# Kernel optimization log

Hardware: AMD Instinct MI355X
Metric: run time of the kernel (lower is better)

Reference implementation:

```python
import jax, jax.numpy as jnp
import numpy as np

B, S, DIM, H = 2, 2048, 1024, 16
DK = DIM // H  # 64
NEG = -10000000000.0


def setup_inputs() -> dict:
    key = jax.random.key(0)
    k1, k2, k3, k4, k5, k6 = jax.random.split(key, 6)
    dec_xs = jax.random.normal(k1, (B, S, DIM), dtype=jnp.float32)
    enc_xs = jax.random.normal(k2, (B, S, DIM), dtype=jnp.float32)
    mask = jax.random.randint(k3, (B, S, S), 0, 2, dtype=jnp.int32)
    # torch Linear weights: out = x @ W.T, bias=False
    sc = 1.0 / np.sqrt(DIM)
    Wq = jax.random.normal(k4, (DIM, DIM), dtype=jnp.float32) * sc
    Wkv = jax.random.normal(k5, (2 * DIM, DIM), dtype=jnp.float32) * sc
    Wo = jax.random.normal(k6, (DIM, DIM), dtype=jnp.float32) * sc
    return {"dec_xs": dec_xs, "enc_xs": enc_xs, "Wq": Wq, "Wkv": Wkv, "Wo": Wo, "mask": mask}


def reference(dec_xs, enc_xs, Wq, Wkv, Wo, mask):
    b, s, dim = enc_xs.shape
    qs = dec_xs @ Wq.T                      # [b,s,dim]  (dropout inactive in eval)
    kv = enc_xs @ Wkv.T                     # [b,s,2*dim]
    ks, vs = jnp.split(kv, 2, axis=-1)
    # head layout: view(b, s, dk, h) -- heads LAST, as in the original
    qs = qs.reshape(b, s, DK, H)
    ks = ks.reshape(b, s, DK, H)
    vs = vs.reshape(b, s, DK, H)
    scores = jnp.einsum('bqdh,bkdh->bqkh', qs, ks) / np.sqrt(DK)
    scores = jnp.where(mask[..., None] == 0, NEG, scores)
    weights = jax.nn.softmax(scores, axis=-2)  # softmax over key axis
    out = jnp.einsum('bqkh,bkdh->bqdh', weights, vs).reshape(b, s, dim)
    return out @ Wo.T
```

## Files before the change

### kernel.cpp

```cpp
#include <hip/hip_runtime.h>
#include <hip/hip_bf16.h>

#define BB 2
#define SS 2048
#define DIMM 1024
#define HH 16
#define DKK 64
#define QSCALE 0.18033688011112042592f

using bf16 = __hip_bfloat16;
typedef __attribute__((ext_vector_type(8))) short v8s;
typedef __attribute__((ext_vector_type(4))) short v4s;
typedef __attribute__((ext_vector_type(4))) float f32x4;
typedef __attribute__((ext_vector_type(16))) float f32x16;

__device__ __forceinline__ void cvt4(const float* __restrict__ s,
                                     bf16* __restrict__ d, int idx) {
  const float4 f = ((const float4*)s)[idx];
  bf16 t[4] = {__float2bfloat16(f.x), __float2bfloat16(f.y),
               __float2bfloat16(f.z), __float2bfloat16(f.w)};
  *(v4s*)(d + (size_t)idx * 4) = *(const v4s*)t;
}

__device__ __forceinline__ int cvt_pk_bf16(float lo, float hi) {
  int r;
  asm("v_cvt_pk_bf16_f32 %0, %1, %2" : "=v"(r) : "v"(lo), "v"(hi));
  return r;
}

__global__ __launch_bounds__(256) void convert_pack_kernel(
    const float* __restrict__ dec, const float* __restrict__ enc,
    const float* __restrict__ Wq, const float* __restrict__ Wkv,
    const float* __restrict__ Wo, const int* __restrict__ mask,
    bf16* __restrict__ decb, bf16* __restrict__ encb, bf16* __restrict__ Wqb,
    bf16* __restrict__ Wkvb, bf16* __restrict__ Wob,
    unsigned long long* __restrict__ mp) {
  const int gid = blockIdx.x * 256 + threadIdx.x;
  const int NT = 256 * 1024;
#pragma unroll
  for (int i = 0; i < 4; ++i) cvt4(dec, decb, gid + i * NT);
#pragma unroll
  for (int i = 0; i < 4; ++i) cvt4(enc, encb, gid + i * NT);
  cvt4(Wq, Wqb, gid);
#pragma unroll
  for (int i = 0; i < 2; ++i) cvt4(Wkv, Wkvb, gid + i * NT);
  {
    const int n = gid >> 8;
    const int c4 = (gid & 255) * 4;
    const int h = c4 >> 6, d0 = c4 & 63;
    const float* src = Wo + (size_t)n * DIMM + h;
    bf16 t[4];
#pragma unroll
    for (int i2 = 0; i2 < 4; ++i2)
      t[i2] = __float2bfloat16(src[(d0 + i2) * 16]);
    *(v4s*)(Wob + (size_t)n * DIMM + c4) = *(const v4s*)t;
  }
  const int lane = threadIdx.x & 63;
  const int wave_id = gid >> 6;
  for (int i = 0; i < 32; ++i) {
    const size_t w = (size_t)wave_id * 32 + i;
    const unsigned long long bm = __ballot(mask[w * 64 + lane] != 0);
    if (lane == 0) {
      const int bb = (int)(w >> 16);
      const int qq = (int)((w >> 5) & 2047);
      const int kc = (int)(w & 31);
      mp[((size_t)bb * 32 + kc) * SS + qq] = bm;
    }
  }
}

__global__ __launch_bounds__(256) void proj_gemm_kernel(
    const bf16* __restrict__ decb, const bf16* __restrict__ encb,
    const bf16* __restrict__ Wqb, const bf16* __restrict__ Wkvb,
    bf16* __restrict__ Qr, bf16* __restrict__ Kr, bf16* __restrict__ Vt) {
  __shared__ __align__(16) bf16 As[128][72];
  __shared__ __align__(16) bf16 Bs[128][72];
  const int t = threadIdx.x;
  const int wave = t >> 6, lane = t & 63;
  const int quad = lane >> 4, l15 = lane & 15;
  const int wm = (wave >> 1) * 64, wn = (wave & 1) * 64;
  const int bx = blockIdx.x;
  const int kind = bx >> 3;
  const int g = bx & 7;
  const int m0 = blockIdx.y * 128;

  const int sr = t >> 2;
  const int sc = (t & 3) * 16;
  const int voff = (kind == 2) ? DIMM : 0;
  const int wr0 = sr * 16 + g * 2 + voff;
  const int wr1 = sr * 16 + g * 2 + 1 + voff;

  const bf16* arow0;
  const bf16* arow1;
  const bf16* brow0;
  const bf16* brow1;
  if (kind == 0) {
    arow0 = decb + (size_t)(m0 + sr) * DIMM;
    arow1 = decb + (size_t)(m0 + sr + 64) * DIMM;
    brow0 = Wqb + (size_t)wr0 * DIMM;
    brow1 = Wqb + (size_t)wr1 * DIMM;
  } else if (kind == 1) {
    arow0 = encb + (size_t)(m0 + sr) * DIMM;
    arow1 = encb + (size_t)(m0 + sr + 64) * DIMM;
    brow0 = Wkvb + (size_t)wr0 * DIMM;
    brow1 = Wkvb + (size_t)wr1 * DIMM;
  } else {
    arow0 = Wkvb + (size_t)wr0 * DIMM;
    arow1 = Wkvb + (size_t)wr1 * DIMM;
    brow0 = encb + (size_t)(m0 + sr) * DIMM;
    brow1 = encb + (size_t)(m0 + sr + 64) * DIMM;
  }

  v8s apf[4], bpf[4];
  auto loadAB = [&](int kc) {
    apf[0] = ((const v8s*)(arow0 + kc + sc))[0];
    apf[1] = ((const v8s*)(arow0 + kc + sc))[1];
    apf[2] = ((const v8s*)(arow1 + kc + sc))[0];
    apf[3] = ((const v8s*)(arow1 + kc + sc))[1];
    bpf[0] = ((const v8s*)(brow0 + kc + sc))[0];
    bpf[1] = ((const v8s*)(brow0 + kc + sc))[1];
    bpf[2] = ((const v8s*)(brow1 + kc + sc))[0];
    bpf[3] = ((const v8s*)(brow1 + kc + sc))[1];
  };

  f32x4 acc[4][4] = {};
  loadAB(0);

  for (int kc = 0; kc < DIMM; kc += 64) {
    __syncthreads();
    *(v8s*)&As[sr][sc] = apf[0];
    *(v8s*)&As[sr][sc + 8] = apf[1];
    *(v8s*)&As[sr + 64][sc] = apf[2];
    *(v8s*)&As[sr + 64][sc + 8] = apf[3];
    *(v8s*)&Bs[sr][sc] = bpf[0];
    *(v8s*)&Bs[sr][sc + 8] = bpf[1];
    *(v8s*)&Bs[sr + 64][sc] = bpf[2];
    *(v8s*)&Bs[sr + 64][sc + 8] = bpf[3];
    if (kc + 64 < DIMM) loadAB(kc + 64);
    __syncthreads();
#pragma unroll
    for (int ks = 0; ks < 2; ++ks) {
      v8s af[4], bfr[4];
#pragma unroll
      for (int i = 0; i < 4; ++i)
        af[i] = *(const v8s*)&As[wm + i * 16 + l15][ks * 32 + quad * 8];
#pragma unroll
      for (int j = 0; j < 4; ++j)
        bfr[j] = *(const v8s*)&Bs[wn + j * 16 + l15][ks * 32 + quad * 8];
#pragma unroll
      for (int i = 0; i < 4; ++i)
#pragma unroll
        for (int j = 0; j < 4; ++j)
          acc[i][j] = __builtin_amdgcn_mfma_f32_16x16x32_bf16(
              af[i], bfr[j], acc[i][j], 0, 0, 0);
    }
  }

#pragma unroll
  for (int i = 0; i < 4; ++i) {
#pragma unroll
    for (int r = 0; r < 4; ++r) {
      const int mm = wm + i * 16 + quad * 4 + r;
#pragma unroll
      for (int j = 0; j < 4; ++j) {
        const int nn = wn + j * 16 + l15;
        const float v = acc[i][j][r];
        if (kind == 0) {
          Qr[(size_t)(m0 + mm) * DIMM + g * 128 + nn] =
              __float2bfloat16(v * QSCALE);
        } else if (kind == 1) {
          Kr[(size_t)(m0 + mm) * DIMM + g * 128 + nn] = __float2bfloat16(v);
        } else {
          const int h = g * 2 + (mm >> 6), d = mm & 63;
          const int sn = m0 + nn;
          const int b = sn >> 11, s = sn & (SS - 1);
          Vt[(((size_t)b * HH + h) * DKK + d) * SS + s] = __float2bfloat16(v);
        }
      }
    }
  }
}

__global__ __launch_bounds__(256) void out_gemm_kernel(
    const bf16* __restrict__ A, const bf16* __restrict__ W,
    float* __restrict__ out) {
  __shared__ __align__(16) bf16 As[128][72];
  __shared__ __align__(16) bf16 Bs[64][72];
  const int t = threadIdx.x;
  const int wave = t >> 6, lane = t & 63;
  const int quad = lane >> 4, l15 = lane & 15;
  const int wm = (wave >> 1) * 64, wn = (wave & 1) * 32;
  const int n0 = blockIdx.x * 64;
  const int m0 = blockIdx.y * 128;
  const int sr = t >> 2;
  const int sc = (t & 3) * 16;

  v8s ar[4], br[2];
  auto loadA = [&](int kc) {
#pragma unroll
    for (int rr = 0; rr < 2; ++rr) {
      const bf16* p = A + (size_t)(m0 + sr + rr * 64) * DIMM + kc + sc;
#pragma unroll
      for (int i = 0; i < 2; ++i) ar[rr * 2 + i] = ((const v8s*)p)[i];
    }
  };
  auto loadB = [&](int kc) {
    const bf16* p = W + (size_t)(n0 + sr) * DIMM + kc + sc;
#pragma unroll
    for (int i = 0; i < 2; ++i) br[i] = ((const v8s*)p)[i];
  };

  f32x4 acc[4][2] = {};
  loadA(0);
  loadB(0);
  for (int kc = 0; kc < DIMM; kc += 64) {
    __syncthreads();
#pragma unroll
    for (int rr = 0; rr < 2; ++rr) {
      *(v8s*)&As[sr + rr * 64][sc] = ar[rr * 2 + 0];
      *(v8s*)&As[sr + rr * 64][sc + 8] = ar[rr * 2 + 1];
    }
    *(v8s*)&Bs[sr][sc] = br[0];
    *(v8s*)&Bs[sr][sc + 8] = br[1];
    if (kc + 64 < DIMM) {
      loadA(kc + 64);
      loadB(kc + 64);
    }
    __syncthreads();
#pragma unroll
    for (int ks = 0; ks < 2; ++ks) {
      v8s af[4], bfr[2];
#pragma unroll
      for (int i = 0; i < 4; ++i)
        af[i] = *(const v8s*)&As[wm + i * 16 + l15][ks * 32 + quad * 8];
#pragma unroll
      for (int j = 0; j < 2; ++j)
        bfr[j] = *(const v8s*)&Bs[wn + j * 16 + l15][ks * 32 + quad * 8];
#pragma unroll
      for (int i = 0; i < 4; ++i)
#pragma unroll
        for (int j = 0; j < 2; ++j)
          acc[i][j] = __builtin_amdgcn_mfma_f32_16x16x32_bf16(
              af[i], bfr[j], acc[i][j], 0, 0, 0);
    }
  }

#pragma unroll
  for (int i = 0; i < 4; ++i) {
#pragma unroll
    for (int r = 0; r < 4; ++r) {
      const int m = m0 + wm + i * 16 + quad * 4 + r;
#pragma unroll
      for (int j = 0; j < 2; ++j) {
        const int n = n0 + wn + j * 16 + l15;
        out[(size_t)m * DIMM + n] = acc[i][j][r];
      }
    }
  }
}

__global__ __launch_bounds__(256) void attn_kernel(
    const bf16* __restrict__ Qr, const bf16* __restrict__ Kr,
    const bf16* __restrict__ Vt, const unsigned long long* __restrict__ mp,
    bf16* __restrict__ Ar) {
  __shared__ __align__(16) bf16 Ks[2][64][72];
  __shared__ __align__(16) bf16 Vs[2][64][72];

  const int t = threadIdx.x;
  const int wave = t >> 6, lane = t & 63;
  const int l31 = lane & 31, hf = lane >> 5;

  const int bx = blockIdx.x;
  const int xcd = bx & 7, j = bx >> 3;
  const int g = (xcd << 2) | (j & 3);
  const int tile = j >> 2;
  const int hd = g & 15, b = g >> 4;

  const int qw = tile * 128 + wave * 32;
  const size_t bhv = ((size_t)b * HH + hd) * DKK;

  v8s bq[4];
  {
    const bf16* qrow = Qr + ((size_t)(b * SS + qw + l31)) * DIMM + hd * 64;
#pragma unroll
    for (int cs = 0; cs < 4; ++cs)
      bq[cs] = *(const v8s*)(qrow + cs * 16 + 8 * hf);
  }

  v8s vones;
#pragma unroll
  for (int i = 0; i < 8; ++i) vones[i] = (short)0x3F80;

  f32x16 o0 = {}, o1 = {}, ol = {};

  const int r0 = t >> 2;
  const int c0 = (t & 3) * 16;

  auto loadK = [&](int kt, v8s* kr) {
    const bf16* p =
        Kr + ((size_t)(b * SS + kt * 64 + r0)) * DIMM + hd * 64 + c0;
    kr[0] = ((const v8s*)p)[0];
    kr[1] = ((const v8s*)p)[1];
  };
  auto loadV = [&](int kt, v8s* vr) {
    const bf16* p = Vt + (bhv + r0) * SS + kt * 64 + c0;
    vr[0] = ((const v8s*)p)[0];
    vr[1] = ((const v8s*)p)[1];
  };
  auto loadM = [&](int kt) {
    return mp[((size_t)b * 32 + kt) * SS + qw + l31];
  };

  v8s kreg[2], vreg[2];
  loadK(0, kreg);
  loadV(0, vreg);
  *(v8s*)&Ks[0][r0][c0] = kreg[0];
  *(v8s*)&Ks[0][r0][c0 + 8] = kreg[1];
  *(v8s*)&Vs[0][r0][c0] = vreg[0];
  *(v8s*)&Vs[0][r0][c0 + 8] = vreg[1];
  loadK(1, kreg);
  loadV(1, vreg);
  unsigned long long mwcur = loadM(0);

  int p = 0;
  for (int kt = 0; kt < 32; ++kt) {
    __syncthreads();
    if (kt < 31) {
      *(v8s*)&Ks[p ^ 1][r0][c0] = kreg[0];
      *(v8s*)&Ks[p ^ 1][r0][c0 + 8] = kreg[1];
      *(v8s*)&Vs[p ^ 1][r0][c0] = vreg[0];
      *(v8s*)&Vs[p ^ 1][r0][c0 + 8] = vreg[1];
      if (kt < 30) {
        loadK(kt + 2, kreg);
        loadV(kt + 2, vreg);
      }
    }
    unsigned long long mwnext = (kt < 31) ? loadM(kt + 1) : 0ULL;
    const unsigned long long mq = mwcur >> (4 * hf);

    f32x16 st[2];
#pragma unroll
    for (int n = 0; n < 2; ++n) {
      f32x16 s = {};
#pragma unroll
      for (int cs = 0; cs < 4; ++cs) {
        const v8s ak = *(const v8s*)&Ks[p][n * 32 + l31][cs * 16 + 8 * hf];
        s = __builtin_amdgcn_mfma_f32_32x32x16_bf16(ak, bq[cs], s, 0, 0, 0);
      }
      st[n] = s;
    }

    int pd[8][2];
#pragma unroll
    for (int n = 0; n < 2; ++n)
#pragma unroll
      for (int g2 = 0; g2 < 4; ++g2)
#pragma unroll
        for (int jj = 0; jj < 2; ++jj) {
          const int bp = 32 * n + 8 * g2 + 2 * jj;
          const int m = g2 * 4 + 2 * jj;
          const float p0 = ((mq >> bp) & 1)
                               ? __builtin_amdgcn_exp2f(st[n][m])
                               : 0.f;
          const float p1 = ((mq >> (bp + 1)) & 1)
                               ? __builtin_amdgcn_exp2f(st[n][m + 1])
                               : 0.f;
          pd[n * 4 + g2][jj] = cvt_pk_bf16(p0, p1);
        }

    v8s af[4];
#pragma unroll
    for (int ks = 0; ks < 4; ++ks) {
      int a0 = pd[2 * ks][0], b0 = pd[2 * ks + 1][0];
      int a1 = pd[2 * ks][1], b1 = pd[2 * ks + 1][1];
      asm("v_permlane32_swap_b32 %0, %1" : "+v"(a0), "+v"(b0));
      asm("v_permlane32_swap_b32 %0, %1" : "+v"(a1), "+v"(b1));
      int4 w;
      w.x = a0;
      w.y = a1;
      w.z = b0;
      w.w = b1;
      af[ks] = *(v8s*)&w;
    }

#pragma unroll
    for (int ks = 0; ks < 4; ++ks) {
      const v8s bv0 = *(const v8s*)&Vs[p][l31][ks * 16 + 8 * hf];
      const v8s bv1 = *(const v8s*)&Vs[p][32 + l31][ks * 16 + 8 * hf];
      o0 = __builtin_amdgcn_mfma_f32_32x32x16_bf16(af[ks], bv0, o0, 0, 0, 0);
      o1 = __builtin_amdgcn_mfma_f32_32x32x16_bf16(af[ks], bv1, o1, 0, 0, 0);
      ol = __builtin_amdgcn_mfma_f32_32x32x16_bf16(af[ks], vones, ol, 0, 0, 0);
    }
    mwcur = mwnext;
    p ^= 1;
  }

#pragma unroll
  for (int m = 0; m < 16; ++m) {
    const float inv = __builtin_amdgcn_rcpf(ol[m]);
    const int q = qw + (m & 3) + 8 * (m >> 2) + 4 * hf;
    const size_t row = (size_t)b * SS + q;
    Ar[row * DIMM + hd * 64 + l31] = __float2bfloat16(o0[m] * inv);
    Ar[row * DIMM + hd * 64 + 32 + l31] = __float2bfloat16(o1[m] * inv);
  }
}

extern "C" void kernel_launch(void* const* d_in, const int* in_sizes, int n_in,
                              void* d_out, int out_size, void* d_ws,
                              size_t ws_size, hipStream_t stream) {
  const float* dec = (const float*)d_in[0];
  const float* enc = (const float*)d_in[1];
  const float* Wq = (const float*)d_in[2];
  const float* Wkv = (const float*)d_in[3];
  const float* Wo = (const float*)d_in[4];
  const int* mask = (const int*)d_in[5];
  float* out = (float*)d_out;

  bf16* decb = (bf16*)d_out;
  bf16* Wqb = (bf16*)((char*)d_out + ((size_t)2 * SS * DIMM * 2));

  char* ws = (char*)d_ws;
  size_t off = 0;
  bf16* encb = (bf16*)(ws + off);
  bf16* Ar = (bf16*)(ws + off);   off += (size_t)2 * SS * DIMM * 2;
  bf16* Wkvb = (bf16*)(ws + off); off += (size_t)2 * DIMM * DIMM * 2;
  bf16* Wob = (bf16*)(ws + off);  off += (size_t)DIMM * DIMM * 2;
  bf16* Qr = (bf16*)(ws + off);   off += (size_t)2 * SS * DIMM * 2;
  bf16* Kr = (bf16*)(ws + off);   off += (size_t)2 * SS * DIMM * 2;
  bf16* Vt = (bf16*)(ws + off);   off += (size_t)2 * SS * DIMM * 2;
  unsigned long long* mp = (unsigned long long*)(ws + off);

  dim3 blk(256);
  convert_pack_kernel<<<dim3(1024), blk, 0, stream>>>(
      dec, enc, Wq, Wkv, Wo, mask, decb, encb, Wqb, Wkvb, Wob, mp);
  proj_gemm_kernel<<<dim3(24, 32), blk, 0, stream>>>(decb, encb, Wqb, Wkvb, Qr,
                                                     Kr, Vt);
  attn_kernel<<<dim3(512), dim3(256), 0, stream>>>(Qr, Kr, Vt, mp, Ar);
  out_gemm_kernel<<<dim3(16, 32), blk, 0, stream>>>(Ar, Wob, out);
}
```

Measured before the change: 245.2 us.

## Split attention key loop across two wave groups and merge partial sums in LDS

Doubles the attention block to 512 threads: waves 0-3 and 4-7 handle even and odd 64-key tiles, each pair of tiles staged together in a double-buffered LDS layout. After the loop, the upper waves write their partial O and row-sum accumulators to shared memory, and the lower waves add them before normalising and storing. This is meant to raise the number of waves per CU and hide latency in a grid of only 512 blocks. The cost is doubled LDS per block, an extra reduction step with two barriers, and fewer registers available per thread.

New measurement: 240.1 us. 2.1% less time.

```diff
diff --git a/kernel.cpp b/kernel.cpp
--- a/kernel.cpp
+++ b/kernel.cpp
@@ -259,16 +259,17 @@
   }
 }
 
-__global__ __launch_bounds__(256) void attn_kernel(
+__global__ __launch_bounds__(512) void attn_kernel(
     const bf16* __restrict__ Qr, const bf16* __restrict__ Kr,
     const bf16* __restrict__ Vt, const unsigned long long* __restrict__ mp,
     bf16* __restrict__ Ar) {
-  __shared__ __align__(16) bf16 Ks[2][64][72];
-  __shared__ __align__(16) bf16 Vs[2][64][72];
+  __shared__ __align__(16) bf16 smem[2][2][2][64][72];
 
   const int t = threadIdx.x;
   const int wave = t >> 6, lane = t & 63;
   const int l31 = lane & 31, hf = lane >> 5;
+  const int qb = wave & 3;
+  const int pr = wave >> 2;
 
   const int bx = blockIdx.x;
   const int xcd = bx & 7, j = bx >> 3;
@@ -276,7 +277,7 @@
   const int tile = j >> 2;
   const int hd = g & 15, b = g >> 4;
 
-  const int qw = tile * 128 + wave * 32;
+  const int qw = tile * 128 + qb * 32;
   const size_t bhv = ((size_t)b * HH + hd) * DKK;
 
   v8s bq[4];
@@ -293,61 +294,64 @@
 
   f32x16 o0 = {}, o1 = {}, ol = {};
 
-  const int r0 = t >> 2;
-  const int c0 = (t & 3) * 16;
-
-  auto loadK = [&](int kt, v8s* kr) {
-    const bf16* p =
-        Kr + ((size_t)(b * SS + kt * 64 + r0)) * DIMM + hd * 64 + c0;
-    kr[0] = ((const v8s*)p)[0];
-    kr[1] = ((const v8s*)p)[1];
-  };
-  auto loadV = [&](int kt, v8s* vr) {
-    const bf16* p = Vt + (bhv + r0) * SS + kt * 64 + c0;
-    vr[0] = ((const v8s*)p)[0];
-    vr[1] = ((const v8s*)p)[1];
+  const int r0 = t >> 3;
+  const int c0 = (t & 7) * 8;
+
+  auto gK = [&](int kt) {
+    return *(const v8s*)(Kr + ((size_t)(b * SS + kt * 64 + r0)) * DIMM +
+                         hd * 64 + c0);
+  };
+  auto gV = [&](int kt) {
+    return *(const v8s*)(Vt + (bhv + r0) * SS + kt * 64 + c0);
   };
   auto loadM = [&](int kt) {
     return mp[((size_t)b * 32 + kt) * SS + qw + l31];
   };
 
-  v8s kreg[2], vreg[2];
-  loadK(0, kreg);
-  loadV(0, vreg);
-  *(v8s*)&Ks[0][r0][c0] = kreg[0];
-  *(v8s*)&Ks[0][r0][c0 + 8] = kreg[1];
-  *(v8s*)&Vs[0][r0][c0] = vreg[0];
-  *(v8s*)&Vs[0][r0][c0 + 8] = vreg[1];
-  loadK(1, kreg);
-  loadV(1, vreg);
-  unsigned long long mwcur = loadM(0);
-
-  int p = 0;
-  for (int kt = 0; kt < 32; ++kt) {
+  {
+    const v8s k0 = gK(0), v0 = gV(0), k1 = gK(1), v1 = gV(1);
+    *(v8s*)&smem[0][0][0][r0][c0] = k0;
+    *(v8s*)&smem[1][0][0][r0][c0] = v0;
+    *(v8s*)&smem[0][1][0][r0][c0] = k1;
+    *(v8s*)&smem[1][1][0][r0][c0] = v1;
+  }
+  v8s kpr[2], vpr[2];
+  kpr[0] = gK(2);
+  vpr[0] = gV(2);
+  kpr[1] = gK(3);
+  vpr[1] = gV(3);
+  unsigned long long mwcur = loadM(pr);
+
+  for (int s = 0; s < 16; ++s) {
     __syncthreads();
-    if (kt < 31) {
-      *(v8s*)&Ks[p ^ 1][r0][c0] = kreg[0];
-      *(v8s*)&Ks[p ^ 1][r0][c0 + 8] = kreg[1];
-      *(v8s*)&Vs[p ^ 1][r0][c0] = vreg[0];
-      *(v8s*)&Vs[p ^ 1][r0][c0 + 8] = vreg[1];
-      if (kt < 30) {
-        loadK(kt + 2, kreg);
-        loadV(kt + 2, vreg);
+    const int nb = (s + 1) & 1;
+    if (s < 15) {
+      *(v8s*)&smem[0][0][nb][r0][c0] = kpr[0];
+      *(v8s*)&smem[1][0][nb][r0][c0] = vpr[0];
+      *(v8s*)&smem[0][1][nb][r0][c0] = kpr[1];
+      *(v8s*)&smem[1][1][nb][r0][c0] = vpr[1];
+      if (s < 14) {
+        kpr[0] = gK(2 * s + 4);
+        vpr[0] = gV(2 * s + 4);
+        kpr[1] = gK(2 * s + 5);
+        vpr[1] = gV(2 * s + 5);
       }
     }
-    unsigned long long mwnext = (kt < 31) ? loadM(kt + 1) : 0ULL;
+    const unsigned long long mwnext = (s < 15) ? loadM(2 * s + 2 + pr) : 0ULL;
     const unsigned long long mq = mwcur >> (4 * hf);
+    const int cb = s & 1;
 
     f32x16 st[2];
 #pragma unroll
     for (int n = 0; n < 2; ++n) {
-      f32x16 s = {};
+      f32x16 sa = {};
 #pragma unroll
       for (int cs = 0; cs < 4; ++cs) {
-        const v8s ak = *(const v8s*)&Ks[p][n * 32 + l31][cs * 16 + 8 * hf];
-        s = __builtin_amdgcn_mfma_f32_32x32x16_bf16(ak, bq[cs], s, 0, 0, 0);
+        const v8s ak =
+            *(const v8s*)&smem[0][pr][cb][n * 32 + l31][cs * 16 + 8 * hf];
+        sa = __builtin_amdgcn_mfma_f32_32x32x16_bf16(ak, bq[cs], sa, 0, 0, 0);
       }
-      st[n] = s;
+      st[n] = sa;
     }
 
     int pd[8][2];
@@ -359,12 +363,11 @@
         for (int jj = 0; jj < 2; ++jj) {
           const int bp = 32 * n + 8 * g2 + 2 * jj;
           const int m = g2 * 4 + 2 * jj;
-          const float p0 = ((mq >> bp) & 1)
-                               ? __builtin_amdgcn_exp2f(st[n][m])
-                               : 0.f;
-          const float p1 = ((mq >> (bp + 1)) & 1)
-                               ? __builtin_amdgcn_exp2f(st[n][m + 1])
-                               : 0.f;
+          const float p0 =
+              ((mq >> bp) & 1) ? __builtin_amdgcn_exp2f(st[n][m]) : 0.f;
+          const float p1 =
+              ((mq >> (bp + 1)) & 1) ? __builtin_amdgcn_exp2f(st[n][m + 1])
+                                     : 0.f;
           pd[n * 4 + g2][jj] = cvt_pk_bf16(p0, p1);
         }
 
@@ -385,23 +388,47 @@
 
 #pragma unroll
     for (int ks = 0; ks < 4; ++ks) {
-      const v8s bv0 = *(const v8s*)&Vs[p][l31][ks * 16 + 8 * hf];
-      const v8s bv1 = *(const v8s*)&Vs[p][32 + l31][ks * 16 + 8 * hf];
+      const v8s bv0 = *(const v8s*)&smem[1][pr][cb][l31][ks * 16 + 8 * hf];
+      const v8s bv1 =
+          *(const v8s*)&smem[1][pr][cb][32 + l31][ks * 16 + 8 * hf];
       o0 = __builtin_amdgcn_mfma_f32_32x32x16_bf16(af[ks], bv0, o0, 0, 0, 0);
       o1 = __builtin_amdgcn_mfma_f32_32x32x16_bf16(af[ks], bv1, o1, 0, 0, 0);
       ol = __builtin_amdgcn_mfma_f32_32x32x16_bf16(af[ks], vones, ol, 0, 0, 0);
     }
     mwcur = mwnext;
-    p ^= 1;
-  }
-
-#pragma unroll
-  for (int m = 0; m < 16; ++m) {
-    const float inv = __builtin_amdgcn_rcpf(ol[m]);
-    const int q = qw + (m & 3) + 8 * (m >> 2) + 4 * hf;
-    const size_t row = (size_t)b * SS + q;
-    Ar[row * DIMM + hd * 64 + l31] = __float2bfloat16(o0[m] * inv);
-    Ar[row * DIMM + hd * 64 + 32 + l31] = __float2bfloat16(o1[m] * inv);
+  }
+
+  __syncthreads();
+  float* scratch = (float*)&smem[0][0][0][0][0];
+  if (wave >= 4) {
+    float* dst = scratch + ((size_t)(wave - 4) * 64 + lane) * 52;
+#pragma unroll
+    for (int i = 0; i < 4; ++i) {
+      f32x4 t0 = {o0[4 * i], o0[4 * i + 1], o0[4 * i + 2], o0[4 * i + 3]};
+      f32x4 t1 = {o1[4 * i], o1[4 * i + 1], o1[4 * i + 2], o1[4 * i + 3]};
+      f32x4 t2 = {ol[4 * i], ol[4 * i + 1], ol[4 * i + 2], ol[4 * i + 3]};
+      *(f32x4*)(dst + 4 * i) = t0;
+      *(f32x4*)(dst + 16 + 4 * i) = t1;
+      *(f32x4*)(dst + 32 + 4 * i) = t2;
+    }
+  }
+  __syncthreads();
+  if (wave < 4) {
+    const float* src = scratch + ((size_t)wave * 64 + lane) * 52;
+#pragma unroll
+    for (int m = 0; m < 16; ++m) {
+      o0[m] += src[m];
+      o1[m] += src[16 + m];
+      ol[m] += src[32 + m];
+    }
+#pragma unroll
+    for (int m = 0; m < 16; ++m) {
+      const float inv = __builtin_amdgcn_rcpf(ol[m]);
+      const int q = qw + (m & 3) + 8 * (m >> 2) + 4 * hf;
+      const size_t row = (size_t)b * SS + q;
+      Ar[row * DIMM + hd * 64 + l31] = __float2bfloat16(o0[m] * inv);
+      Ar[row * DIMM + hd * 64 + 32 + l31] = __float2bfloat16(o1[m] * inv);
+    }
   }
 }
 
@@ -435,6 +462,6 @@
       dec, enc, Wq, Wkv, Wo, mask, decb, encb, Wqb, Wkvb, Wob, mp);
   proj_gemm_kernel<<<dim3(24, 32), blk, 0, stream>>>(decb, encb, Wqb, Wkvb, Qr,
                                                      Kr, Vt);
-  attn_kernel<<<dim3(512), dim3(256), 0, stream>>>(Qr, Kr, Vt, mp, Ar);
+  attn_kernel<<<dim3(512), dim3(512), 0, stream>>>(Qr, Kr, Vt, mp, Ar);
   out_gemm_kernel<<<dim3(16, 32), blk, 0, stream>>>(Ar, Wob, out);
 }
```
